# Performance work log

Hardware: AMD Instinct MI355X
Metric: run time of the kernel (lower is better)

## Reference

```python
import jax, jax.numpy as jnp
import numpy as np

N = 100_000   # nodes
E = 1_600_000 # edges (avg degree 16)
C = 64        # in/out channels
H = 64        # hidden width of pos_nn / attn_nn MLPs


def setup_inputs() -> dict:
    key = jax.random.key(0)
    ks = jax.random.split(key, 16)
    g = lambda k, s, fan: (jax.random.normal(k, s, jnp.float32) / np.float32(np.sqrt(fan)))
    return {
        "x": jax.random.normal(ks[0], (N, C), jnp.float32),
        "pos": jax.random.uniform(ks[1], (N, 2), jnp.float32),
        "edge_index": jax.random.randint(ks[2], (2, E), 0, N, jnp.int32),
        # linear_in (bias=True)
        "W_in": g(ks[3], (C, C), C), "b_in": jnp.zeros((C,), jnp.float32),
        # PointTransformerConv: lin (values), lin_src, lin_dst -- all bias=False in PyG
        "W_lin": g(ks[4], (C, C), C),
        "W_src": g(ks[5], (C, C), C),
        "W_dst": g(ks[6], (C, C), C),
        # pos_nn: MLP([2, 64, C], norm=None, plain_last=False) => Lin+ReLU, Lin+ReLU
        "Wp1": g(ks[7], (2, H), 2), "bp1": jnp.zeros((H,), jnp.float32),
        "Wp2": g(ks[8], (H, C), H), "bp2": jnp.zeros((C,), jnp.float32),
        # attn_nn: MLP([C, 64, C], norm=None, plain_last=False)
        "Wa1": g(ks[9], (C, H), C), "ba1": jnp.zeros((H,), jnp.float32),
        "Wa2": g(ks[10], (H, C), H), "ba2": jnp.zeros((C,), jnp.float32),
        # linear_out (bias=True)
        "W_out": g(ks[11], (C, C), C), "b_out": jnp.zeros((C,), jnp.float32),
    }


def reference(x, pos, edge_index, W_in, b_in, W_lin, W_src, W_dst,
              Wp1, bp1, Wp2, bp2, Wa1, ba1, Wa2, ba2, W_out, b_out):
    src = edge_index[0]  # j (message source)
    dst = edge_index[1]  # i (message target)

    # linear_in + relu
    h = jax.nn.relu(x @ W_in + b_in)                      # [N, C]

    # PointTransformerConv node projections
    a_dst = h @ W_dst                                     # alpha_i term [N, C]
    a_src = h @ W_src                                     # alpha_j term [N, C]
    v = h @ W_lin                                         # values     [N, C]

    # positional encoding delta = pos_nn(pos_i - pos_j)
    dpos = pos[dst] - pos[src]                            # [E, 2]
    delta = jax.nn.relu(jax.nn.relu(dpos @ Wp1 + bp1) @ Wp2 + bp2)  # [E, C]

    # attention logits: attn_nn(alpha_i - alpha_j + delta)
    a = a_dst[dst] - a_src[src] + delta                   # [E, C]
    a = jax.nn.relu(jax.nn.relu(a @ Wa1 + ba1) @ Wa2 + ba2)         # [E, C]

    # per-dst-node, per-channel segment softmax (PyG softmax with 1e-16 eps)
    amax = jax.ops.segment_max(a, dst, num_segments=N)    # [N, C]
    amax = jnp.where(jnp.isfinite(amax), amax, 0.0)
    ex = jnp.exp(a - amax[dst])                           # [E, C]
    denom = jax.ops.segment_sum(ex, dst, num_segments=N)  # [N, C]
    alpha = ex / (denom[dst] + 1e-16)                     # [E, C]

    # weighted scatter-aggregate of (v_j + delta)
    out = jax.ops.segment_sum(alpha * (v[src] + delta), dst, num_segments=N)  # [N, C]

    # linear_out + relu
    return jax.nn.relu(out @ W_out + b_out)
```

## Files before the change

kernel.cpp:

```cpp
#include <hip/hip_runtime.h>

#define N_NODES 100000
#define N_EDGES 1600000
#define NB (N_EDGES / 64)
#define PITCH 68
#define PITCHH 72
#define N_SCAN_BLOCKS ((N_NODES + 1023) / 1024)
#define HIST_BLOCKS (N_EDGES / 256)
#define WCONV_BLOCKS 48
#define NPROJ_BLOCKS ((N_NODES + 63) / 64)

typedef _Float16 half8 __attribute__((ext_vector_type(8)));
typedef float f32x4 __attribute__((ext_vector_type(4)));

__device__ __forceinline__ int wave_c0() {
  return __builtin_amdgcn_readfirstlane((int)((threadIdx.x >> 6) << 4));
}

template<bool RELU, bool BIAS>
__device__ __forceinline__ void wave_gemm16(const float* Alds, int lane, int c0,
                                            const float* __restrict__ W,
                                            const float* __restrict__ bias,
                                            float acc[16]) {
#pragma unroll
  for (int j = 0; j < 16; ++j) acc[j] = BIAS ? bias[c0 + j] : 0.0f;
  const float* arow = Alds + lane * PITCH;
#pragma unroll
  for (int k = 0; k < 64; k += 4) {
    const float4 a4 = *reinterpret_cast<const float4*>(arow + k);
    const float av[4] = {a4.x, a4.y, a4.z, a4.w};
#pragma unroll
    for (int kk = 0; kk < 4; ++kk) {
#pragma unroll
      for (int j = 0; j < 16; ++j)
        acc[j] = fmaf(av[kk], W[(k + kk) * 64 + c0 + j], acc[j]);
    }
  }
  if (RELU) {
#pragma unroll
    for (int j = 0; j < 16; ++j) acc[j] = fmaxf(acc[j], 0.0f);
  }
}

__device__ __forceinline__ void store4x4(float* dst, const float a[16]) {
#pragma unroll
  for (int q = 0; q < 4; ++q)
    *reinterpret_cast<float4*>(dst + q * 4) =
        make_float4(a[q * 4], a[q * 4 + 1], a[q * 4 + 2], a[q * 4 + 3]);
}

__device__ __forceinline__ void store16h(_Float16* dst, const float a[16]) {
  half8 h0, h1;
#pragma unroll
  for (int u = 0; u < 8; ++u) {
    h0[u] = (_Float16)a[u];
    h1[u] = (_Float16)a[8 + u];
  }
  *reinterpret_cast<half8*>(dst) = h0;
  *reinterpret_cast<half8*>(dst + 8) = h1;
}

__global__ __launch_bounds__(256) void prep_kernel(
    const int* __restrict__ ei, int* __restrict__ counts,
    const float* __restrict__ Wp2, const float* __restrict__ Wa1,
    const float* __restrict__ Wa2, _Float16* __restrict__ wt,
    const float* __restrict__ x, const float* __restrict__ W_in,
    const float* __restrict__ b_in, const float* __restrict__ W_lin,
    const float* __restrict__ W_src, const float* __restrict__ W_dst,
    _Float16* __restrict__ adh, _Float16* __restrict__ ash,
    _Float16* __restrict__ vh) {
  __shared__ __align__(16) float A[64 * PITCH];
  const int b = blockIdx.x;
  if (b < HIST_BLOCKS) {
    const int e = b * 256 + threadIdx.x;
    if (e < N_EDGES) atomicAdd(&counts[ei[N_EDGES + e]], 1);
    return;
  }
  if (b < HIST_BLOCKS + WCONV_BLOCKS) {
    const int t = (b - HIST_BLOCKS) * 256 + threadIdx.x;
    if (t < 3 * 4096) {
      const int m = t >> 12, idx = t & 4095;
      const int j = idx >> 6, k = idx & 63;
      const float* W = (m == 0) ? Wp2 : ((m == 1) ? Wa1 : Wa2);
      wt[m * 4096 + j * 64 + k] = (_Float16)W[k * 64 + j];
    }
    return;
  }
  const int tid = threadIdx.x, lane = tid & 63, c0 = wave_c0();
  const int n0 = (b - HIST_BLOCKS - WCONV_BLOCKS) * 64;
#pragma unroll
  for (int i = 0; i < 4; ++i) {
    int idx4 = tid + i * 256;
    int e = idx4 >> 4, k4 = (idx4 & 15) * 4;
    int n = n0 + e;
    float4 val = make_float4(0.f, 0.f, 0.f, 0.f);
    if (n < N_NODES) val = *reinterpret_cast<const float4*>(x + (size_t)n * 64 + k4);
    *reinterpret_cast<float4*>(&A[e * PITCH + k4]) = val;
  }
  __syncthreads();
  float h[16];
  wave_gemm16<true, true>(A, lane, c0, W_in, b_in, h);
  __syncthreads();
  store4x4(&A[lane * PITCH + c0], h);
  __syncthreads();
  float o1[16], o2[16], o3[16];
  wave_gemm16<false, false>(A, lane, c0, W_dst, nullptr, o1);
  wave_gemm16<false, false>(A, lane, c0, W_src, nullptr, o2);
  wave_gemm16<false, false>(A, lane, c0, W_lin, nullptr, o3);
  const int n = n0 + lane;
  if (n < N_NODES) {
    store16h(adh + (size_t)n * 64 + c0, o1);
    store16h(ash + (size_t)n * 64 + c0, o2);
    store16h(vh + (size_t)n * 64 + c0, o3);
  }
}

__global__ __launch_bounds__(1024) void scan1_kernel(const int* __restrict__ counts,
                                                     int* __restrict__ pexcl,
                                                     int* __restrict__ btot) {
  __shared__ int wsum[16];
  const int tid = threadIdx.x, lane = tid & 63, wid = tid >> 6;
  const int idx = blockIdx.x * 1024 + tid;
  const int val = (idx < N_NODES) ? counts[idx] : 0;
  int x = val;
#pragma unroll
  for (int o = 1; o < 64; o <<= 1) {
    int y = __shfl_up(x, o);
    if (lane >= o) x += y;
  }
  if (lane == 63) wsum[wid] = x;
  __syncthreads();
  if (wid == 0) {
    int s = (lane < 16) ? wsum[lane] : 0;
#pragma unroll
    for (int o = 1; o < 16; o <<= 1) {
      int y = __shfl_up(s, o);
      if (lane >= o) s += y;
    }
    if (lane < 16) wsum[lane] = s;
  }
  __syncthreads();
  const int woff = (wid > 0) ? wsum[wid - 1] : 0;
  const int incl = woff + x;
  if (idx < N_NODES) pexcl[idx] = incl - val;
  if (tid == 1023) btot[blockIdx.x] = incl;
}

__global__ __launch_bounds__(64) void scan2_kernel(int* __restrict__ btot) {
  const int lane = threadIdx.x;
  int carry = 0;
  for (int base = 0; base < N_SCAN_BLOCKS; base += 64) {
    const int ii = base + lane;
    const int v = (ii < N_SCAN_BLOCKS) ? btot[ii] : 0;
    int x = v;
#pragma unroll
    for (int o = 1; o < 64; o <<= 1) {
      int y = __shfl_up(x, o);
      if (lane >= o) x += y;
    }
    if (ii < N_SCAN_BLOCKS) btot[ii] = carry + x - v;
    carry += __shfl(x, 63);
  }
}

__global__ __launch_bounds__(256) void scatter_kernel(const int* __restrict__ ei,
                                                      int* __restrict__ pexcl,
                                                      const int* __restrict__ btot,
                                                      int2* __restrict__ order2) {
  int e = blockIdx.x * 256 + threadIdx.x;
  if (e < N_EDGES) {
    int s = ei[e];
    int d = ei[N_EDGES + e];
    int p = atomicAdd(&pexcl[d], 1) + btot[d >> 10];
    order2[p] = make_int2(s, d);
  }
}

__device__ __forceinline__ void mfma3(const _Float16* aL, int w, int g, int a,
                                      const _Float16* __restrict__ Wt,
                                      const float* __restrict__ bias,
                                      f32x4 acc[4]) {
  const half8 A0 = *reinterpret_cast<const half8*>(aL + (16 * w + a) * PITCHH + 8 * g);
  const half8 A1 = *reinterpret_cast<const half8*>(aL + (16 * w + a) * PITCHH + 32 + 8 * g);
#pragma unroll
  for (int t = 0; t < 4; ++t) {
    const half8 B0 = *reinterpret_cast<const half8*>(Wt + (16 * t + a) * 64 + 8 * g);
    const half8 B1 = *reinterpret_cast<const half8*>(Wt + (16 * t + a) * 64 + 32 + 8 * g);
    const float bv = bias[16 * t + a];
    f32x4 c = {bv, bv, bv, bv};
    c = __builtin_amdgcn_mfma_f32_16x16x32_f16(A0, B0, c, 0, 0, 0);
    c = __builtin_amdgcn_mfma_f32_16x16x32_f16(A1, B1, c, 0, 0, 0);
    acc[t] = c;
  }
}

__global__ __launch_bounds__(256) void edge_kernel(
    const int2* __restrict__ order2, const float* __restrict__ pos,
    const float* __restrict__ Wp1, const float* __restrict__ bp1,
    const _Float16* __restrict__ wt, const float* __restrict__ bp2,
    const float* __restrict__ ba1, const float* __restrict__ ba2,
    const _Float16* __restrict__ adh, const _Float16* __restrict__ ash,
    const _Float16* __restrict__ vh, float* __restrict__ num,
    float* __restrict__ den, float* __restrict__ pbuf,
    int* __restrict__ headd, int* __restrict__ taild) {
  __shared__ __align__(16) _Float16 s_act[64 * PITCHH];
  __shared__ __align__(16) _Float16 s_v[64 * PITCHH];
  __shared__ __align__(16) _Float16 s_p[64 * PITCHH];
  __shared__ int s_segd[64];
  const int tid = threadIdx.x, lane = tid & 63, w = tid >> 6;
  const int g = lane >> 4, a = lane & 15, c0 = w * 16;
  const int i = blockIdx.x * 64 + lane;
#pragma unroll
  for (int q = tid; q < 576; q += 256)
    *reinterpret_cast<int4*>(&s_p[q * 8]) = make_int4(0, 0, 0, 0);
  if (tid < 64) s_segd[tid] = -1;
  const int2 sd = order2[i];
  const int d = sd.y;
  const int er = 16 * w + (lane >> 2);
  const int p = lane & 3;
  const int2 sd2 = order2[blockIdx.x * 64 + er];
  const int s2 = sd2.x, d2 = sd2.y;
  const _Float16* adr = adh + (size_t)d2 * 64 + 16 * p;
  const _Float16* asr = ash + (size_t)s2 * 64 + 16 * p;
  const _Float16* vr  = vh  + (size_t)s2 * 64 + 16 * p;
  const half8 ad0 = *reinterpret_cast<const half8*>(adr);
  const half8 ad1 = *reinterpret_cast<const half8*>(adr + 8);
  const half8 as0 = *reinterpret_cast<const half8*>(asr);
  const half8 as1 = *reinterpret_cast<const half8*>(asr + 8);
  const half8 v0  = *reinterpret_cast<const half8*>(vr);
  const half8 v1  = *reinterpret_cast<const half8*>(vr + 8);
  int dm1 = -1, dp1 = -1;
  if (lane == 0 && i > 0) dm1 = order2[i - 1].y;
  if (lane == 63 && i + 1 < N_EDGES) dp1 = order2[i + 1].y;
  dm1 = __shfl(dm1, 0);
  dp1 = __shfl(dp1, 63);
  const int dprev = __shfl_up(d, 1);
  const bool head = (lane == 0) || (d != dprev);
  const unsigned long long hb = __ballot(head);
  const unsigned long long maskle =
      (lane == 63) ? ~0ull : ((1ull << (lane + 1)) - 1ull);
  const int sid = __popcll(hb & maskle) - 1;
  const int nseg = __popcll(hb);
  const int d0 = __shfl(d, 0), dl = __shfl(d, 63);
  {
    const float2 pd = reinterpret_cast<const float2*>(pos)[d2];
    const float2 ps = reinterpret_cast<const float2*>(pos)[s2];
    const float dx = pd.x - ps.x, dy = pd.y - ps.y;
    half8 h0, h1;
#pragma unroll
    for (int u = 0; u < 8; ++u) {
      const int j0 = 16 * p + u, j1 = 16 * p + 8 + u;
      h0[u] = (_Float16)fmaxf(fmaf(dx, Wp1[j0], fmaf(dy, Wp1[64 + j0], bp1[j0])), 0.f);
      h1[u] = (_Float16)fmaxf(fmaf(dx, Wp1[j1], fmaf(dy, Wp1[64 + j1], bp1[j1])), 0.f);
    }
    *reinterpret_cast<half8*>(&s_act[er * PITCHH + 16 * p]) = h0;
    *reinterpret_cast<half8*>(&s_act[er * PITCHH + 16 * p + 8]) = h1;
  }
  f32x4 acc[4];
  mfma3(s_act, w, g, a, wt, bp2, acc);
#pragma unroll
  for (int t = 0; t < 4; ++t)
#pragma unroll
    for (int r = 0; r < 4; ++r)
      s_act[(16 * w + 4 * g + r) * PITCHH + 16 * t + a] =
          (_Float16)fmaxf(acc[t][r], 0.f);
  {
    const half8 dl0 = *reinterpret_cast<const half8*>(&s_act[er * PITCHH + 16 * p]);
    const half8 dl1 = *reinterpret_cast<const half8*>(&s_act[er * PITCHH + 16 * p + 8]);
    *reinterpret_cast<half8*>(&s_act[er * PITCHH + 16 * p]) = ad0 - as0 + dl0;
    *reinterpret_cast<half8*>(&s_act[er * PITCHH + 16 * p + 8]) = ad1 - as1 + dl1;
    *reinterpret_cast<half8*>(&s_v[er * PITCHH + 16 * p]) = v0 + dl0;
    *reinterpret_cast<half8*>(&s_v[er * PITCHH + 16 * p + 8]) = v1 + dl1;
  }
  mfma3(s_act, w, g, a, wt + 4096, ba1, acc);
#pragma unroll
  for (int t = 0; t < 4; ++t)
#pragma unroll
    for (int r = 0; r < 4; ++r)
      s_act[(16 * w + 4 * g + r) * PITCHH + 16 * t + a] =
          (_Float16)fmaxf(acc[t][r], 0.f);
  mfma3(s_act, w, g, a, wt + 2 * 4096, ba2, acc);
#pragma unroll
  for (int t = 0; t < 4; ++t)
#pragma unroll
    for (int r = 0; r < 4; ++r)
      s_act[(16 * w + 4 * g + r) * PITCHH + 16 * t + a] =
          (_Float16)__expf(fmaxf(acc[t][r], 0.f));
  __syncthreads();
  const half8 e0 = *reinterpret_cast<const half8*>(&s_act[lane * PITCHH + c0]);
  const half8 e1 = *reinterpret_cast<const half8*>(&s_act[lane * PITCHH + c0 + 8]);
  const half8 vd0 = *reinterpret_cast<const half8*>(&s_v[lane * PITCHH + c0]);
  const half8 vd1 = *reinterpret_cast<const half8*>(&s_v[lane * PITCHH + c0 + 8]);
  const half8 m0 = e0 * vd0;
  const half8 m1 = e1 * vd1;
  __syncthreads();
#pragma unroll
  for (int j = 0; j < 8; ++j) {
    s_act[(c0 + j) * PITCHH + lane] = e0[j];
    s_act[(c0 + 8 + j) * PITCHH + lane] = e1[j];
    s_v[(c0 + j) * PITCHH + lane] = m0[j];
    s_v[(c0 + 8 + j) * PITCHH + lane] = m1[j];
  }
  if (w == 0) {
    s_p[sid * PITCHH + lane] = (_Float16)1.0f;
    if (head) s_segd[sid] = d;
  }
  if (tid == 0) {
    const bool ts0 = (dm1 != d0);
    const bool te0 = (nseg > 1) || (dp1 != d0);
    headd[blockIdx.x] = ts0 ? -1 : (te0 ? d0 : -2);
    taild[blockIdx.x] = (dp1 != dl) ? -1 : dl;
  }
  __syncthreads();
  if (16 * w < nseg) {
    const half8 PA0 = *reinterpret_cast<const half8*>(&s_p[(16 * w + a) * PITCHH + 8 * g]);
    const half8 PA1 = *reinterpret_cast<const half8*>(&s_p[(16 * w + a) * PITCHH + 32 + 8 * g]);
    f32x4 accN[4], accD[4];
#pragma unroll
    for (int t = 0; t < 4; ++t) {
      const half8 Bd0 = *reinterpret_cast<const half8*>(&s_act[(16 * t + a) * PITCHH + 8 * g]);
      const half8 Bd1 = *reinterpret_cast<const half8*>(&s_act[(16 * t + a) * PITCHH + 32 + 8 * g]);
      f32x4 cd = {0.f, 0.f, 0.f, 0.f};
      cd = __builtin_amdgcn_mfma_f32_16x16x32_f16(PA0, Bd0, cd, 0, 0, 0);
      cd = __builtin_amdgcn_mfma_f32_16x16x32_f16(PA1, Bd1, cd, 0, 0, 0);
      accD[t] = cd;
      const half8 Bn0 = *reinterpret_cast<const half8*>(&s_v[(16 * t + a) * PITCHH + 8 * g]);
      const half8 Bn1 = *reinterpret_cast<const half8*>(&s_v[(16 * t + a) * PITCHH + 32 + 8 * g]);
      f32x4 cn = {0.f, 0.f, 0.f, 0.f};
      cn = __builtin_amdgcn_mfma_f32_16x16x32_f16(PA0, Bn0, cn, 0, 0, 0);
      cn = __builtin_amdgcn_mfma_f32_16x16x32_f16(PA1, Bn1, cn, 0, 0, 0);
      accN[t] = cn;
    }
#pragma unroll
    for (int r = 0; r < 4; ++r) {
      const int seg = 16 * w + 4 * g + r;
      const int dseg = s_segd[seg];
      if (dseg >= 0) {
        const bool ts = (seg > 0) || (dm1 != dseg);
        const bool te = (seg < nseg - 1) || (dp1 != dseg);
        if (ts && te) {
          float* np = num + (size_t)dseg * 64 + a;
          float* dp_ = den + (size_t)dseg * 64 + a;
#pragma unroll
          for (int t = 0; t < 4; ++t) {
            np[16 * t] = accN[t][r];
            dp_[16 * t] = accD[t][r];
          }
        } else {
          const int slot = (!ts && te) ? 0 : 1;
          float* pb = pbuf + (size_t)blockIdx.x * 256 + slot * 128 + a;
#pragma unroll
          for (int t = 0; t < 4; ++t) {
            pb[16 * t] = accN[t][r];
            pb[64 + 16 * t] = accD[t][r];
          }
        }
      }
    }
  }
}

__global__ __launch_bounds__(128) void finish_kernel(
    const float* __restrict__ pbuf, const int* __restrict__ headd,
    const int* __restrict__ taild, float* __restrict__ num,
    float* __restrict__ den) {
  const int b = blockIdx.x + 1;
  const int t = taild[b - 1];
  if (t < 0) return;
  const int ch = threadIdx.x & 63, arr = threadIdx.x >> 6;
  const int h = headd[b];
  const float tv = pbuf[(size_t)(b - 1) * 256 + 128 + arr * 64 + ch];
  float* dst = (arr ? den : num) + (size_t)t * 64 + ch;
  if (h == t) {
    const float hv = pbuf[(size_t)b * 256 + arr * 64 + ch];
    if (headd[b - 1] != -2) {
      *dst = tv + hv;
    } else {
      atomicAdd(dst, tv + hv);
    }
  } else {
    atomicAdd(dst, tv);
  }
}

__global__ __launch_bounds__(256) void out_kernel(
    const float* __restrict__ num, const float* __restrict__ den,
    const float* __restrict__ W_out, const float* __restrict__ b_out,
    float* __restrict__ out) {
  __shared__ __align__(16) float A[64 * PITCH];
  const int tid = threadIdx.x, lane = tid & 63, c0 = wave_c0();
  const int n0 = blockIdx.x * 64;
#pragma unroll
  for (int i = 0; i < 4; ++i) {
    int idx4 = tid + i * 256;
    int e = idx4 >> 4, k4 = (idx4 & 15) * 4;
    int n = n0 + e;
    float4 val = make_float4(0.f, 0.f, 0.f, 0.f);
    if (n < N_NODES) {
      float4 nu = *reinterpret_cast<const float4*>(num + (size_t)n * 64 + k4);
      float4 de = *reinterpret_cast<const float4*>(den + (size_t)n * 64 + k4);
      val.x = nu.x / (de.x + 1e-16f);
      val.y = nu.y / (de.y + 1e-16f);
      val.z = nu.z / (de.z + 1e-16f);
      val.w = nu.w / (de.w + 1e-16f);
    }
    *reinterpret_cast<float4*>(&A[e * PITCH + k4]) = val;
  }
  __syncthreads();
  float o[16];
  wave_gemm16<true, true>(A, lane, c0, W_out, b_out, o);
  const int n = n0 + lane;
  if (n < N_NODES) store4x4(out + (size_t)n * 64 + c0, o);
}

extern "C" void kernel_launch(void* const* d_in, const int* in_sizes, int n_in,
                              void* d_out, int out_size, void* d_ws,
                              size_t ws_size, hipStream_t stream) {
  const float* x     = (const float*)d_in[0];
  const float* pos   = (const float*)d_in[1];
  const int*   ei    = (const int*)d_in[2];
  const float* W_in  = (const float*)d_in[3];
  const float* b_in  = (const float*)d_in[4];
  const float* W_lin = (const float*)d_in[5];
  const float* W_src = (const float*)d_in[6];
  const float* W_dst = (const float*)d_in[7];
  const float* Wp1   = (const float*)d_in[8];
  const float* bp1   = (const float*)d_in[9];
  const float* Wp2   = (const float*)d_in[10];
  const float* bp2   = (const float*)d_in[11];
  const float* Wa1   = (const float*)d_in[12];
  const float* ba1   = (const float*)d_in[13];
  const float* Wa2   = (const float*)d_in[14];
  const float* ba2   = (const float*)d_in[15];
  const float* W_out = (const float*)d_in[16];
  const float* b_out = (const float*)d_in[17];
  float* out = (float*)d_out;

  const size_t NC = (size_t)N_NODES * 64;
  _Float16* adh = (_Float16*)d_ws;
  _Float16* ash = adh + NC;
  _Float16* vh  = ash + NC;
  float* num = (float*)(vh + NC);
  float* den = num + NC;
  int* counts = (int*)(den + NC);
  int* pexcl  = counts + N_NODES;
  int* btot   = pexcl + N_NODES;
  int2* order2 = (int2*)(btot + 128);
  float* pbuf  = (float*)(order2 + N_EDGES);
  int* headd   = (int*)(pbuf + (size_t)NB * 256);
  int* taild   = headd + NB;
  _Float16* wt = (_Float16*)(taild + NB);

  hipMemsetAsync(num, 0, (2 * NC + N_NODES) * sizeof(float), stream);

  prep_kernel<<<HIST_BLOCKS + WCONV_BLOCKS + NPROJ_BLOCKS, 256, 0, stream>>>(
      ei, counts, Wp2, Wa1, Wa2, wt, x, W_in, b_in, W_lin, W_src, W_dst,
      adh, ash, vh);
  scan1_kernel<<<N_SCAN_BLOCKS, 1024, 0, stream>>>(counts, pexcl, btot);
  scan2_kernel<<<1, 64, 0, stream>>>(btot);
  scatter_kernel<<<(N_EDGES + 255) / 256, 256, 0, stream>>>(ei, pexcl, btot, order2);

  edge_kernel<<<NB, 256, 0, stream>>>(
      order2, pos, Wp1, bp1, wt, bp2, ba1, ba2, adh, ash, vh, num, den,
      pbuf, headd, taild);
  finish_kernel<<<NB - 1, 128, 0, stream>>>(pbuf, headd, taild, num, den);
  out_kernel<<<(N_NODES + 63) / 64, 256, 0, stream>>>(num, den, W_out, b_out, out);
}
```

Measured before the change: 763.7 us.

## Fuse scatter with node projection and store normalized fp16 aggregates

The node projection GEMM moves out of the histogram kernel and is interleaved with the edge scatter in one launch, four scatter blocks per projection block, so the two phases overlap. The edge kernel now writes the normalized result num/den as fp16 into a single buffer instead of two fp32 num/den arrays. Only nodes whose segments span blocks fall back to atomic fp32 accumulation, marked by a per-node flag. This cuts edge-kernel and out-kernel memory traffic, but adds a flag array, a branch in out_kernel and fp16 rounding of the aggregate.

```diff
diff --git a/kernel.cpp b/kernel.cpp
--- a/kernel.cpp
+++ b/kernel.cpp
@@ -60,34 +60,95 @@
   *reinterpret_cast<half8*>(dst + 8) = h1;
 }
 
-__global__ __launch_bounds__(256) void prep_kernel(
+__global__ __launch_bounds__(256) void histwconv_kernel(
     const int* __restrict__ ei, int* __restrict__ counts,
     const float* __restrict__ Wp2, const float* __restrict__ Wa1,
-    const float* __restrict__ Wa2, _Float16* __restrict__ wt,
+    const float* __restrict__ Wa2, _Float16* __restrict__ wt) {
+  const int b = blockIdx.x;
+  if (b < HIST_BLOCKS) {
+    const int e = b * 256 + threadIdx.x;
+    if (e < N_EDGES) atomicAdd(&counts[ei[N_EDGES + e]], 1);
+    return;
+  }
+  const int t = (b - HIST_BLOCKS) * 256 + threadIdx.x;
+  if (t < 3 * 4096) {
+    const int m = t >> 12, idx = t & 4095;
+    const int j = idx >> 6, k = idx & 63;
+    const float* W = (m == 0) ? Wp2 : ((m == 1) ? Wa1 : Wa2);
+    wt[m * 4096 + j * 64 + k] = (_Float16)W[k * 64 + j];
+  }
+}
+
+__global__ __launch_bounds__(1024) void scan1_kernel(const int* __restrict__ counts,
+                                                     int* __restrict__ pexcl,
+                                                     int* __restrict__ btot) {
+  __shared__ int wsum[16];
+  const int tid = threadIdx.x, lane = tid & 63, wid = tid >> 6;
+  const int idx = blockIdx.x * 1024 + tid;
+  const int val = (idx < N_NODES) ? counts[idx] : 0;
+  int x = val;
+#pragma unroll
+  for (int o = 1; o < 64; o <<= 1) {
+    int y = __shfl_up(x, o);
+    if (lane >= o) x += y;
+  }
+  if (lane == 63) wsum[wid] = x;
+  __syncthreads();
+  if (wid == 0) {
+    int s = (lane < 16) ? wsum[lane] : 0;
+#pragma unroll
+    for (int o = 1; o < 16; o <<= 1) {
+      int y = __shfl_up(s, o);
+      if (lane >= o) s += y;
+    }
+    if (lane < 16) wsum[lane] = s;
+  }
+  __syncthreads();
+  const int woff = (wid > 0) ? wsum[wid - 1] : 0;
+  const int incl = woff + x;
+  if (idx < N_NODES) pexcl[idx] = incl - val;
+  if (tid == 1023) btot[blockIdx.x] = incl;
+}
+
+__global__ __launch_bounds__(64) void scan2_kernel(int* __restrict__ btot) {
+  const int lane = threadIdx.x;
+  int carry = 0;
+  for (int base = 0; base < N_SCAN_BLOCKS; base += 64) {
+    const int ii = base + lane;
+    const int v = (ii < N_SCAN_BLOCKS) ? btot[ii] : 0;
+    int x = v;
+#pragma unroll
+    for (int o = 1; o < 64; o <<= 1) {
+      int y = __shfl_up(x, o);
+      if (lane >= o) x += y;
+    }
+    if (ii < N_SCAN_BLOCKS) btot[ii] = carry + x - v;
+    carry += __shfl(x, 63);
+  }
+}
+
+__global__ __launch_bounds__(256) void scatnproj_kernel(
+    const int* __restrict__ ei, int* __restrict__ pexcl,
+    const int* __restrict__ btot, int2* __restrict__ order2,
     const float* __restrict__ x, const float* __restrict__ W_in,
     const float* __restrict__ b_in, const float* __restrict__ W_lin,
     const float* __restrict__ W_src, const float* __restrict__ W_dst,
     _Float16* __restrict__ adh, _Float16* __restrict__ ash,
     _Float16* __restrict__ vh) {
   __shared__ __align__(16) float A[64 * PITCH];
-  const int b = blockIdx.x;
-  if (b < HIST_BLOCKS) {
-    const int e = b * 256 + threadIdx.x;
-    if (e < N_EDGES) atomicAdd(&counts[ei[N_EDGES + e]], 1);
+  const int b = blockIdx.x, grp = b / 5, pos = b % 5;
+  if (pos < 4) {
+    const int e = (4 * grp + pos) * 256 + threadIdx.x;
+    if (e < N_EDGES) {
+      const int s = ei[e];
+      const int d = ei[N_EDGES + e];
+      const int p = atomicAdd(&pexcl[d], 1) + btot[d >> 10];
+      order2[p] = make_int2(s, d);
+    }
     return;
   }
-  if (b < HIST_BLOCKS + WCONV_BLOCKS) {
-    const int t = (b - HIST_BLOCKS) * 256 + threadIdx.x;
-    if (t < 3 * 4096) {
-      const int m = t >> 12, idx = t & 4095;
-      const int j = idx >> 6, k = idx & 63;
-      const float* W = (m == 0) ? Wp2 : ((m == 1) ? Wa1 : Wa2);
-      wt[m * 4096 + j * 64 + k] = (_Float16)W[k * 64 + j];
-    }
-    return;
-  }
   const int tid = threadIdx.x, lane = tid & 63, c0 = wave_c0();
-  const int n0 = (b - HIST_BLOCKS - WCONV_BLOCKS) * 64;
+  const int n0 = grp * 64;
 #pragma unroll
   for (int i = 0; i < 4; ++i) {
     int idx4 = tid + i * 256;
@@ -115,67 +176,6 @@
   }
 }
 
-__global__ __launch_bounds__(1024) void scan1_kernel(const int* __restrict__ counts,
-                                                     int* __restrict__ pexcl,
-                                                     int* __restrict__ btot) {
-  __shared__ int wsum[16];
-  const int tid = threadIdx.x, lane = tid & 63, wid = tid >> 6;
-  const int idx = blockIdx.x * 1024 + tid;
-  const int val = (idx < N_NODES) ? counts[idx] : 0;
-  int x = val;
-#pragma unroll
-  for (int o = 1; o < 64; o <<= 1) {
-    int y = __shfl_up(x, o);
-    if (lane >= o) x += y;
-  }
-  if (lane == 63) wsum[wid] = x;
-  __syncthreads();
-  if (wid == 0) {
-    int s = (lane < 16) ? wsum[lane] : 0;
-#pragma unroll
-    for (int o = 1; o < 16; o <<= 1) {
-      int y = __shfl_up(s, o);
-      if (lane >= o) s += y;
-    }
-    if (lane < 16) wsum[lane] = s;
-  }
-  __syncthreads();
-  const int woff = (wid > 0) ? wsum[wid - 1] : 0;
-  const int incl = woff + x;
-  if (idx < N_NODES) pexcl[idx] = incl - val;
-  if (tid == 1023) btot[blockIdx.x] = incl;
-}
-
-__global__ __launch_bounds__(64) void scan2_kernel(int* __restrict__ btot) {
-  const int lane = threadIdx.x;
-  int carry = 0;
-  for (int base = 0; base < N_SCAN_BLOCKS; base += 64) {
-    const int ii = base + lane;
-    const int v = (ii < N_SCAN_BLOCKS) ? btot[ii] : 0;
-    int x = v;
-#pragma unroll
-    for (int o = 1; o < 64; o <<= 1) {
-      int y = __shfl_up(x, o);
-      if (lane >= o) x += y;
-    }
-    if (ii < N_SCAN_BLOCKS) btot[ii] = carry + x - v;
-    carry += __shfl(x, 63);
-  }
-}
-
-__global__ __launch_bounds__(256) void scatter_kernel(const int* __restrict__ ei,
-                                                      int* __restrict__ pexcl,
-                                                      const int* __restrict__ btot,
-                                                      int2* __restrict__ order2) {
-  int e = blockIdx.x * 256 + threadIdx.x;
-  if (e < N_EDGES) {
-    int s = ei[e];
-    int d = ei[N_EDGES + e];
-    int p = atomicAdd(&pexcl[d], 1) + btot[d >> 10];
-    order2[p] = make_int2(s, d);
-  }
-}
-
 __device__ __forceinline__ void mfma3(const _Float16* aL, int w, int g, int a,
                                       const _Float16* __restrict__ Wt,
                                       const float* __restrict__ bias,
@@ -200,9 +200,9 @@
     const _Float16* __restrict__ wt, const float* __restrict__ bp2,
     const float* __restrict__ ba1, const float* __restrict__ ba2,
     const _Float16* __restrict__ adh, const _Float16* __restrict__ ash,
-    const _Float16* __restrict__ vh, float* __restrict__ num,
-    float* __restrict__ den, float* __restrict__ pbuf,
-    int* __restrict__ headd, int* __restrict__ taild) {
+    const _Float16* __restrict__ vh, _Float16* __restrict__ rh,
+    float* __restrict__ pbuf, int* __restrict__ headd,
+    int* __restrict__ taild) {
   __shared__ __align__(16) _Float16 s_act[64 * PITCHH];
   __shared__ __align__(16) _Float16 s_v[64 * PITCHH];
   __shared__ __align__(16) _Float16 s_p[64 * PITCHH];
@@ -339,13 +339,10 @@
         const bool ts = (seg > 0) || (dm1 != dseg);
         const bool te = (seg < nseg - 1) || (dp1 != dseg);
         if (ts && te) {
-          float* np = num + (size_t)dseg * 64 + a;
-          float* dp_ = den + (size_t)dseg * 64 + a;
-#pragma unroll
-          for (int t = 0; t < 4; ++t) {
-            np[16 * t] = accN[t][r];
-            dp_[16 * t] = accD[t][r];
-          }
+          _Float16* rp = rh + (size_t)dseg * 64 + a;
+#pragma unroll
+          for (int t = 0; t < 4; ++t)
+            rp[16 * t] = (_Float16)(accN[t][r] / (accD[t][r] + 1e-16f));
         } else {
           const int slot = (!ts && te) ? 0 : 1;
           float* pb = pbuf + (size_t)blockIdx.x * 256 + slot * 128 + a;
@@ -360,51 +357,74 @@
   }
 }
 
-__global__ __launch_bounds__(128) void finish_kernel(
+__global__ __launch_bounds__(64) void finish_kernel(
     const float* __restrict__ pbuf, const int* __restrict__ headd,
     const int* __restrict__ taild, float* __restrict__ num,
-    float* __restrict__ den) {
+    float* __restrict__ den, int* __restrict__ flags,
+    _Float16* __restrict__ rh) {
   const int b = blockIdx.x + 1;
   const int t = taild[b - 1];
   if (t < 0) return;
-  const int ch = threadIdx.x & 63, arr = threadIdx.x >> 6;
+  const int ch = threadIdx.x;
   const int h = headd[b];
-  const float tv = pbuf[(size_t)(b - 1) * 256 + 128 + arr * 64 + ch];
-  float* dst = (arr ? den : num) + (size_t)t * 64 + ch;
-  if (h == t) {
-    const float hv = pbuf[(size_t)b * 256 + arr * 64 + ch];
-    if (headd[b - 1] != -2) {
-      *dst = tv + hv;
-    } else {
-      atomicAdd(dst, tv + hv);
-    }
+  const float tvN = pbuf[(size_t)(b - 1) * 256 + 128 + ch];
+  const float tvD = pbuf[(size_t)(b - 1) * 256 + 128 + 64 + ch];
+  if (h == t && headd[b - 1] != -2) {
+    const float hvN = pbuf[(size_t)b * 256 + ch];
+    const float hvD = pbuf[(size_t)b * 256 + 64 + ch];
+    rh[(size_t)t * 64 + ch] = (_Float16)((tvN + hvN) / (tvD + hvD + 1e-16f));
+  } else if (h == t) {
+    const float hvN = pbuf[(size_t)b * 256 + ch];
+    const float hvD = pbuf[(size_t)b * 256 + 64 + ch];
+    atomicAdd(&num[(size_t)t * 64 + ch], tvN + hvN);
+    atomicAdd(&den[(size_t)t * 64 + ch], tvD + hvD);
+    if (ch == 0) flags[t] = 1;
   } else {
-    atomicAdd(dst, tv);
+    atomicAdd(&num[(size_t)t * 64 + ch], tvN);
+    atomicAdd(&den[(size_t)t * 64 + ch], tvD);
+    if (ch == 0) flags[t] = 1;
   }
 }
 
 __global__ __launch_bounds__(256) void out_kernel(
+    const _Float16* __restrict__ rh, const int* __restrict__ flags,
     const float* __restrict__ num, const float* __restrict__ den,
     const float* __restrict__ W_out, const float* __restrict__ b_out,
     float* __restrict__ out) {
   __shared__ __align__(16) float A[64 * PITCH];
   const int tid = threadIdx.x, lane = tid & 63, c0 = wave_c0();
   const int n0 = blockIdx.x * 64;
-#pragma unroll
-  for (int i = 0; i < 4; ++i) {
-    int idx4 = tid + i * 256;
-    int e = idx4 >> 4, k4 = (idx4 & 15) * 4;
-    int n = n0 + e;
-    float4 val = make_float4(0.f, 0.f, 0.f, 0.f);
+  {
+    const int e = tid >> 2, q = tid & 3;
+    const int n = n0 + e;
+    float vv[16];
+#pragma unroll
+    for (int u = 0; u < 16; ++u) vv[u] = 0.f;
     if (n < N_NODES) {
-      float4 nu = *reinterpret_cast<const float4*>(num + (size_t)n * 64 + k4);
-      float4 de = *reinterpret_cast<const float4*>(den + (size_t)n * 64 + k4);
-      val.x = nu.x / (de.x + 1e-16f);
-      val.y = nu.y / (de.y + 1e-16f);
-      val.z = nu.z / (de.z + 1e-16f);
-      val.w = nu.w / (de.w + 1e-16f);
-    }
-    *reinterpret_cast<float4*>(&A[e * PITCH + k4]) = val;
+      if (__builtin_expect(flags[n], 0)) {
+#pragma unroll
+        for (int u = 0; u < 4; ++u) {
+          const float4 nu = *reinterpret_cast<const float4*>(num + (size_t)n * 64 + q * 16 + 4 * u);
+          const float4 de = *reinterpret_cast<const float4*>(den + (size_t)n * 64 + q * 16 + 4 * u);
+          vv[4 * u + 0] = nu.x / (de.x + 1e-16f);
+          vv[4 * u + 1] = nu.y / (de.y + 1e-16f);
+          vv[4 * u + 2] = nu.z / (de.z + 1e-16f);
+          vv[4 * u + 3] = nu.w / (de.w + 1e-16f);
+        }
+      } else {
+        const half8 r0 = *reinterpret_cast<const half8*>(rh + (size_t)n * 64 + q * 16);
+        const half8 r1 = *reinterpret_cast<const half8*>(rh + (size_t)n * 64 + q * 16 + 8);
+#pragma unroll
+        for (int u = 0; u < 8; ++u) {
+          vv[u] = (float)r0[u];
+          vv[8 + u] = (float)r1[u];
+        }
+      }
+    }
+#pragma unroll
+    for (int u = 0; u < 4; ++u)
+      *reinterpret_cast<float4*>(&A[e * PITCH + q * 16 + 4 * u]) =
+          make_float4(vv[4 * u], vv[4 * u + 1], vv[4 * u + 2], vv[4 * u + 3]);
   }
   __syncthreads();
   float o[16];
@@ -440,29 +460,37 @@
   _Float16* adh = (_Float16*)d_ws;
   _Float16* ash = adh + NC;
   _Float16* vh  = ash + NC;
-  float* num = (float*)(vh + NC);
-  float* den = num + NC;
-  int* counts = (int*)(den + NC);
-  int* pexcl  = counts + N_NODES;
-  int* btot   = pexcl + N_NODES;
-  int2* order2 = (int2*)(btot + 128);
-  float* pbuf  = (float*)(order2 + N_EDGES);
-  int* headd   = (int*)(pbuf + (size_t)NB * 256);
-  int* taild   = headd + NB;
-  _Float16* wt = (_Float16*)(taild + NB);
-
-  hipMemsetAsync(num, 0, (2 * NC + N_NODES) * sizeof(float), stream);
-
-  prep_kernel<<<HIST_BLOCKS + WCONV_BLOCKS + NPROJ_BLOCKS, 256, 0, stream>>>(
-      ei, counts, Wp2, Wa1, Wa2, wt, x, W_in, b_in, W_lin, W_src, W_dst,
-      adh, ash, vh);
+  float* num    = (float*)(vh + NC);
+  float* den    = num + NC;
+  int* counts   = (int*)(den + NC);
+  int* flags    = counts + N_NODES;
+  _Float16* rh  = (_Float16*)(flags + N_NODES);
+  int* pexcl    = (int*)(rh + NC);
+  int* btot     = pexcl + N_NODES;
+  int2* order2  = (int2*)(btot + 128);
+  float* pbuf   = (float*)(order2 + N_EDGES);
+  int* headd    = (int*)(pbuf + (size_t)NB * 256);
+  int* taild    = headd + NB;
+  _Float16* wt  = (_Float16*)(taild + NB);
+
+  hipMemsetAsync(num, 0,
+                 2 * NC * sizeof(float) + 2 * N_NODES * sizeof(int) +
+                     NC * sizeof(_Float16),
+                 stream);
+
+  histwconv_kernel<<<HIST_BLOCKS + WCONV_BLOCKS, 256, 0, stream>>>(
+      ei, counts, Wp2, Wa1, Wa2, wt);
   scan1_kernel<<<N_SCAN_BLOCKS, 1024, 0, stream>>>(counts, pexcl, btot);
   scan2_kernel<<<1, 64, 0, stream>>>(btot);
-  scatter_kernel<<<(N_EDGES + 255) / 256, 256, 0, stream>>>(ei, pexcl, btot, order2);
+  scatnproj_kernel<<<5 * NPROJ_BLOCKS, 256, 0, stream>>>(
+      ei, pexcl, btot, order2, x, W_in, b_in, W_lin, W_src, W_dst,
+      adh, ash, vh);
 
   edge_kernel<<<NB, 256, 0, stream>>>(
-      order2, pos, Wp1, bp1, wt, bp2, ba1, ba2, adh, ash, vh, num, den,
+      order2, pos, Wp1, bp1, wt, bp2, ba1, ba2, adh, ash, vh, rh,
       pbuf, headd, taild);
-  finish_kernel<<<NB - 1, 128, 0, stream>>>(pbuf, headd, taild, num, den);
-  out_kernel<<<(N_NODES + 63) / 64, 256, 0, stream>>>(num, den, W_out, b_out, out);
-}
+  finish_kernel<<<NB - 1, 64, 0, stream>>>(pbuf, headd, taild, num, den,
+                                           flags, rh);
+  out_kernel<<<(N_NODES + 63) / 64, 256, 0, stream>>>(rh, flags, num, den,
+                                                      W_out, b_out, out);
+}
```

Result: faster. 676.0 us (-11.5%).
